# Kernel tuning notes

Measured on AMD Instinct MI355X. Metric: run time of the kernel, lower is better.

## Reference

```python
import jax, jax.numpy as jnp
import numpy as np


def setup_inputs() -> dict:
    key = jax.random.key(0)
    ks = jax.random.split(key, 6)
    B, S, D, H, K = 16384, 16, 256, 128, 32
    s1 = 1.0 / np.sqrt(D)
    s2 = 1.0 / np.sqrt(H)
    s3 = 1.0 / np.sqrt(K)
    return {
        "x": jax.random.normal(ks[0], (B, D), jnp.float32),
        "W1": jax.random.normal(ks[1], (S, D, H), jnp.float32) * s1,
        "b1": jnp.zeros((S, H), jnp.float32),
        "W2": jax.random.normal(ks[2], (S, H, D), jnp.float32) * s2,
        "b2": jnp.zeros((S, D), jnp.float32),
        "Wc1": jax.random.normal(ks[3], (S, D, K), jnp.float32) * s1,
        "bc1": jnp.zeros((S, K), jnp.float32),
        "Wc2": jax.random.normal(ks[4], (S, K), jnp.float32) * s3,
        "bc2": jnp.zeros((S,), jnp.float32),
        "lam": jnp.ones((S,), jnp.float32) / S,  # lambda_weights init = 1/n_sources
    }


def reference(x, W1, b1, W2, b2, Wc1, bc1, Wc2, bc2, lam):
    # Batched per-source 2-layer MLP: [B,D] x [S,D,H] -> [B,S,H]
    h = jax.nn.relu(jnp.einsum("bd,sdh->bsh", x, W1) + b1[None])
    outs = jnp.einsum("bsh,shd->bsd", h, W2) + b2[None]            # [B,S,D]
    # Confidence net on each source output
    ch = jax.nn.relu(jnp.einsum("bsd,sdk->bsk", outs, Wc1) + bc1[None])
    conf = jax.nn.sigmoid(jnp.einsum("bsk,sk->bs", ch, Wc2) + bc2[None])  # [B,S]
    # Weighted, normalized combination
    cw = lam[None, :] * conf                                        # [B,S]
    cw = cw / (cw.sum(axis=1, keepdims=True) + 1e-6)
    out = jnp.einsum("bsd,bs->bd", outs, cw)                        # [B,D]
    return out
```

## Files before the change

kernel.cpp:

```cpp
#include <hip/hip_runtime.h>
#include <math.h>

#define S_N 16
#define D_N 256
#define H_N 128
#define K_N 32
#define BT  64
#define B_N 16384

typedef __attribute__((ext_vector_type(8))) short bf16x8;
typedef __attribute__((ext_vector_type(4))) float f32x4;

#define MFMA(a, b, c) __builtin_amdgcn_mfma_f32_16x16x32_bf16(a, b, c, 0, 0, 0)

static __device__ __forceinline__ unsigned short f2bf(float f) {
  union { float f; unsigned u; } v; v.f = f;
  unsigned r = v.u + 0x7FFFu + ((v.u >> 16) & 1u);
  return (unsigned short)(r >> 16);
}

__global__ __launch_bounds__(256)
void lsi_prep(const float* __restrict__ W1, const float* __restrict__ W2,
              const float* __restrict__ Wc1, const float* __restrict__ b2,
              const float* __restrict__ bc1,
              unsigned short* __restrict__ W1t,
              unsigned short* __restrict__ W2t,
              unsigned short* __restrict__ Wft,
              float* __restrict__ bcf)
{
  const int bid = blockIdx.x;
  if (bid < 1024) {
    __shared__ float t[32][33];
    const float* src; unsigned short* dst; int R, C, r0, c0;
    if (bid < 512) {
      int s = bid >> 5, tt = bid & 31;
      R = 256; C = 128; r0 = (tt >> 2) * 32; c0 = (tt & 3) * 32;
      src = W1 + (size_t)s * 256 * 128; dst = W1t + (size_t)s * 128 * 256;
    } else {
      int s = (bid - 512) >> 5, tt = (bid - 512) & 31;
      R = 128; C = 256; r0 = (tt >> 3) * 32; c0 = (tt & 7) * 32;
      src = W2 + (size_t)s * 128 * 256; dst = W2t + (size_t)s * 256 * 128;
    }
    int li = threadIdx.x >> 5, lj = threadIdx.x & 31;
    #pragma unroll
    for (int i = 0; i < 4; ++i)
      t[li + i * 8][lj] = src[(size_t)(r0 + li + i * 8) * C + c0 + lj];
    __syncthreads();
    #pragma unroll
    for (int i = 0; i < 4; ++i)
      dst[(size_t)(c0 + li + i * 8) * R + r0 + lj] = f2bf(t[lj][li + i * 8]);
    return;
  }
  const int q  = bid - 1024;
  const int s  = q >> 3, hb = q & 7;
  const int t  = threadIdx.x;
  const int hh = hb * 16 + (t >> 4);
  const int kb = (t & 15) * 2;
  const float* w2r = W2 + ((size_t)s * H_N + hh) * D_N;
  const float* wc1 = Wc1 + (size_t)s * D_N * K_N;
  float a0 = 0.f, a1 = 0.f;
  for (int d = 0; d < D_N; ++d) {
    float wv = w2r[d];
    a0 = fmaf(wv, wc1[d * K_N + kb], a0);
    a1 = fmaf(wv, wc1[d * K_N + kb + 1], a1);
  }
  Wft[((size_t)s * K_N + kb) * H_N + hh]     = f2bf(a0);
  Wft[((size_t)s * K_N + kb + 1) * H_N + hh] = f2bf(a1);
  if (hb == 0 && t < K_N) {
    float a = bc1[s * K_N + t];
    for (int d = 0; d < D_N; ++d)
      a = fmaf(b2[s * D_N + d], wc1[d * K_N + t], a);
    bcf[s * K_N + t] = a;
  }
}

template<int SPLIT>
__global__ __launch_bounds__(512, 2)
void lsi_main(const float* __restrict__ x,
              const float* __restrict__ b1,
              const float* __restrict__ b2,
              const float* __restrict__ Wc2,
              const float* __restrict__ bc2,
              const float* __restrict__ lam,
              const unsigned short* __restrict__ W1t,
              const unsigned short* __restrict__ W2t,
              const unsigned short* __restrict__ Wft,
              const float* __restrict__ bcf,
              float* __restrict__ outp,
              float* __restrict__ pwsum)
{
  __shared__ unsigned short x_lds[BT * D_N];
  __shared__ unsigned short h_lds[BT * H_N];
  __shared__ float cw_lds[BT];
  __shared__ float wsum_lds[BT];

  const int tid = threadIdx.x;
  const int w   = tid >> 6;
  const int l   = tid & 63;
  const int rA  = l & 15;
  const int g   = l >> 4;
  const int k8  = g * 8;

  int rb, half, s0, ns;
  if (SPLIT) { rb = blockIdx.x & 255; half = blockIdx.x >> 8; s0 = half * 8; ns = 8; }
  else       { rb = blockIdx.x;       half = 0;               s0 = 0;        ns = 16; }
  const int b0 = rb * BT;

  {
    int row = tid >> 3;
    int c0  = (tid & 7) * 32;
    const float* xr = x + (size_t)(b0 + row) * D_N + c0;
    #pragma unroll
    for (int cc = 0; cc < 4; ++cc) {
      float4 f0 = *(const float4*)(xr + cc * 8);
      float4 f1 = *(const float4*)(xr + cc * 8 + 4);
      bf16x8 u;
      u[0] = f2bf(f0.x); u[1] = f2bf(f0.y); u[2] = f2bf(f0.z); u[3] = f2bf(f0.w);
      u[4] = f2bf(f1.x); u[5] = f2bf(f1.y); u[6] = f2bf(f1.z); u[7] = f2bf(f1.w);
      unsigned off = (unsigned)(row * 512 + (c0 + cc * 8) * 2) ^ (unsigned)((row & 7) << 4);
      *(bf16x8*)((char*)x_lds + off) = u;
    }
  }
  if (tid < BT) wsum_lds[tid] = 0.f;

  f32x4 out_acc[2][4];
  f32x4 acc2[2][4];
  #pragma unroll
  for (int a = 0; a < 2; ++a)
    #pragma unroll
    for (int b = 0; b < 4; ++b)
      out_acc[a][b] = (f32x4){0.f, 0.f, 0.f, 0.f};

  __syncthreads();

  for (int si = 0; si < ns; ++si) {
    const int s = s0 + si;

    f32x4 acc1[4];
    #pragma unroll
    for (int rt = 0; rt < 4; ++rt) acc1[rt] = (f32x4){0.f, 0.f, 0.f, 0.f};
    {
      const unsigned short* B1 = W1t + ((size_t)s * H_N + w * 16 + rA) * D_N + k8;
      #pragma unroll
      for (int ks = 0; ks < 8; ++ks) {
        bf16x8 bfr = *(const bf16x8*)(B1 + ks * 32);
        #pragma unroll
        for (int rt = 0; rt < 4; ++rt) {
          int row = rt * 16 + rA;
          unsigned off = (unsigned)(row * 512 + (ks * 32 + k8) * 2) ^ (unsigned)((row & 7) << 4);
          bf16x8 afr = *(const bf16x8*)((const char*)x_lds + off);
          acc1[rt] = MFMA(afr, bfr, acc1[rt]);
        }
      }
    }
    if (si > 0) {
      #pragma unroll
      for (int rt = 0; rt < 4; ++rt) {
        f32x4 c4 = *(const f32x4*)&cw_lds[rt * 16 + g * 4];
        #pragma unroll
        for (int i = 0; i < 4; ++i) {
          out_acc[0][rt][i] += c4[i] * acc2[0][rt][i];
          out_acc[1][rt][i] += c4[i] * acc2[1][rt][i];
        }
      }
    }
    {
      const float b1v = b1[s * H_N + w * 16 + rA];
      #pragma unroll
      for (int rt = 0; rt < 4; ++rt)
        #pragma unroll
        for (int i = 0; i < 4; ++i) {
          float v = fmaxf(acc1[rt][i] + b1v, 0.f);
          int row = rt * 16 + g * 4 + i;
          unsigned off = (unsigned)(row * 256 + (w * 16 + rA) * 2) ^ (unsigned)((row & 7) << 4);
          *(unsigned short*)((char*)h_lds + off) = f2bf(v);
        }
    }
    __syncthreads();

    if (w < 4) {
      f32x4 acc3[2];
      acc3[0] = (f32x4){0.f, 0.f, 0.f, 0.f};
      acc3[1] = (f32x4){0.f, 0.f, 0.f, 0.f};
      const unsigned short* Bf = Wft + ((size_t)s * K_N + rA) * H_N + k8;
      #pragma unroll
      for (int ks = 0; ks < 4; ++ks) {
        int row = w * 16 + rA;
        unsigned off = (unsigned)(row * 256 + (ks * 32 + k8) * 2) ^ (unsigned)((row & 7) << 4);
        bf16x8 afr = *(const bf16x8*)((const char*)h_lds + off);
        acc3[0] = MFMA(afr, *(const bf16x8*)(Bf + ks * 32), acc3[0]);
        acc3[1] = MFMA(afr, *(const bf16x8*)(Bf + 16 * H_N + ks * 32), acc3[1]);
      }
      const float bcf0 = bcf[s * K_N + rA],      bcf1 = bcf[s * K_N + 16 + rA];
      const float wc20 = Wc2[s * K_N + rA],      wc21 = Wc2[s * K_N + 16 + rA];
      float pz[4];
      #pragma unroll
      for (int i = 0; i < 4; ++i)
        pz[i] = fmaxf(acc3[0][i] + bcf0, 0.f) * wc20 +
                fmaxf(acc3[1][i] + bcf1, 0.f) * wc21;
      #pragma unroll
      for (int m = 1; m < 16; m <<= 1)
        #pragma unroll
        for (int i = 0; i < 4; ++i)
          pz[i] += __shfl_xor(pz[i], m);
      if (rA == 0) {
        const float lam_s = lam[s], bc2_s = bc2[s];
        #pragma unroll
        for (int i = 0; i < 4; ++i) {
          float cv = lam_s / (1.f + __expf(-(pz[i] + bc2_s)));
          cw_lds[w * 16 + g * 4 + i] = cv;
          wsum_lds[w * 16 + g * 4 + i] += cv;
        }
      }
    }

    #pragma unroll
    for (int a = 0; a < 2; ++a)
      #pragma unroll
      for (int b = 0; b < 4; ++b)
        acc2[a][b] = (f32x4){0.f, 0.f, 0.f, 0.f};
    {
      const unsigned short* B2 = W2t + ((size_t)s * D_N + w * 32 + rA) * H_N + k8;
      #pragma unroll
      for (int ks = 0; ks < 4; ++ks) {
        bf16x8 afr[4];
        #pragma unroll
        for (int rt = 0; rt < 4; ++rt) {
          int row = rt * 16 + rA;
          unsigned off = (unsigned)(row * 256 + (ks * 32 + k8) * 2) ^ (unsigned)((row & 7) << 4);
          afr[rt] = *(const bf16x8*)((const char*)h_lds + off);
        }
        #pragma unroll
        for (int ct = 0; ct < 2; ++ct) {
          bf16x8 bfr = *(const bf16x8*)(B2 + ct * 16 * H_N + ks * 32);
          #pragma unroll
          for (int rt = 0; rt < 4; ++rt)
            acc2[ct][rt] = MFMA(afr[rt], bfr, acc2[ct][rt]);
        }
      }
    }
    {
      float b2v0 = b2[s * D_N + w * 32 + rA];
      float b2v1 = b2[s * D_N + w * 32 + 16 + rA];
      #pragma unroll
      for (int rt = 0; rt < 4; ++rt)
        #pragma unroll
        for (int i = 0; i < 4; ++i) {
          acc2[0][rt][i] += b2v0;
          acc2[1][rt][i] += b2v1;
        }
    }
    __syncthreads();
  }

  #pragma unroll
  for (int rt = 0; rt < 4; ++rt) {
    f32x4 c4 = *(const f32x4*)&cw_lds[rt * 16 + g * 4];
    #pragma unroll
    for (int i = 0; i < 4; ++i) {
      out_acc[0][rt][i] += c4[i] * acc2[0][rt][i];
      out_acc[1][rt][i] += c4[i] * acc2[1][rt][i];
    }
  }
  if (SPLIT) {
    float* po = outp + (size_t)half * B_N * D_N;
    #pragma unroll
    for (int rt = 0; rt < 4; ++rt)
      #pragma unroll
      for (int i = 0; i < 4; ++i) {
        int row = rt * 16 + g * 4 + i;
        po[(size_t)(b0 + row) * D_N + w * 32 + rA]      = out_acc[0][rt][i];
        po[(size_t)(b0 + row) * D_N + w * 32 + 16 + rA] = out_acc[1][rt][i];
      }
    if (tid < BT) pwsum[half * B_N + b0 + tid] = wsum_lds[tid];
  } else {
    #pragma unroll
    for (int rt = 0; rt < 4; ++rt) {
      f32x4 w4 = *(const f32x4*)&wsum_lds[rt * 16 + g * 4];
      #pragma unroll
      for (int i = 0; i < 4; ++i) {
        int row = rt * 16 + g * 4 + i;
        float winv = 1.f / (w4[i] + 1e-6f);
        outp[(size_t)(b0 + row) * D_N + w * 32 + rA]      = out_acc[0][rt][i] * winv;
        outp[(size_t)(b0 + row) * D_N + w * 32 + 16 + rA] = out_acc[1][rt][i] * winv;
      }
    }
  }
}

__global__ __launch_bounds__(256)
void lsi_combine(const float* __restrict__ pout, const float* __restrict__ pwsum,
                 float* __restrict__ out)
{
  size_t i4 = ((size_t)blockIdx.x * 256 + threadIdx.x) * 4;
  int row = (int)(i4 >> 8);
  f32x4 a = *(const f32x4*)(pout + i4);
  f32x4 b = *(const f32x4*)(pout + (size_t)B_N * D_N + i4);
  float ws = pwsum[row] + pwsum[B_N + row];
  float inv = 1.f / (ws + 1e-6f);
  f32x4 r;
  #pragma unroll
  for (int i = 0; i < 4; ++i) r[i] = (a[i] + b[i]) * inv;
  *(f32x4*)(out + i4) = r;
}

extern "C" void kernel_launch(void* const* d_in, const int* in_sizes, int n_in,
                              void* d_out, int out_size, void* d_ws, size_t ws_size,
                              hipStream_t stream) {
  const float* x   = (const float*)d_in[0];
  const float* W1  = (const float*)d_in[1];
  const float* b1  = (const float*)d_in[2];
  const float* W2  = (const float*)d_in[3];
  const float* b2  = (const float*)d_in[4];
  const float* Wc1 = (const float*)d_in[5];
  const float* bc1 = (const float*)d_in[6];
  const float* Wc2 = (const float*)d_in[7];
  const float* bc2 = (const float*)d_in[8];
  const float* lam = (const float*)d_in[9];
  float* out = (float*)d_out;

  unsigned short* W1t = (unsigned short*)d_ws;
  unsigned short* W2t = W1t + (size_t)S_N * H_N * D_N;
  unsigned short* Wft = W2t + (size_t)S_N * D_N * H_N;
  float* bcf   = (float*)(Wft + (size_t)S_N * K_N * H_N);
  float* pwsum = bcf + S_N * K_N;
  float* pout  = pwsum + 2 * B_N;
  size_t need = (size_t)((char*)(pout + (size_t)2 * B_N * D_N) - (char*)d_ws);

  lsi_prep<<<dim3(1152), dim3(256), 0, stream>>>(W1, W2, Wc1, b2, bc1,
                                                 W1t, W2t, Wft, bcf);
  if (ws_size >= need) {
    lsi_main<1><<<dim3(512), dim3(512), 0, stream>>>(x, b1, b2, Wc2, bc2, lam,
                                                     W1t, W2t, Wft, bcf, pout, pwsum);
    lsi_combine<<<dim3((B_N * D_N) / 1024), dim3(256), 0, stream>>>(pout, pwsum, out);
  } else {
    lsi_main<0><<<dim3(256), dim3(512), 0, stream>>>(x, b1, b2, Wc2, bc2, lam,
                                                     W1t, W2t, Wft, bcf, out, nullptr);
  }
}
```

Before: 133.2 us.

## Halve batch tile to 32 rows with 256-thread blocks and wider per-wave column tiles

The batch tile drops from 64 to 32 rows and blocks shrink from 8 to 4 waves, with the grid doubled. Each wave now covers twice as many H and D columns: 32 H columns in the first GEMM and 64 D columns in the second. The confidence net runs on 2 waves instead of 4. The goal is smaller blocks and more of them, giving finer scheduling and more resident blocks per CU. The cost is that every bf16 weight matrix is streamed from cache by twice as many blocks, and each B fragment is reused across fewer row tiles.

```diff
diff --git a/kernel.cpp b/kernel.cpp
--- a/kernel.cpp
+++ b/kernel.cpp
@@ -5,7 +5,7 @@
 #define D_N 256
 #define H_N 128
 #define K_N 32
-#define BT  64
+#define BT  32
 #define B_N 16384
 
 typedef __attribute__((ext_vector_type(8))) short bf16x8;
@@ -75,7 +75,7 @@
 }
 
 template<int SPLIT>
-__global__ __launch_bounds__(512, 2)
+__global__ __launch_bounds__(256, 4)
 void lsi_main(const float* __restrict__ x,
               const float* __restrict__ b1,
               const float* __restrict__ b2,
@@ -102,7 +102,7 @@
   const int k8  = g * 8;
 
   int rb, half, s0, ns;
-  if (SPLIT) { rb = blockIdx.x & 255; half = blockIdx.x >> 8; s0 = half * 8; ns = 8; }
+  if (SPLIT) { rb = blockIdx.x & 511; half = blockIdx.x >> 9; s0 = half * 8; ns = 8; }
   else       { rb = blockIdx.x;       half = 0;               s0 = 0;        ns = 16; }
   const int b0 = rb * BT;
 
@@ -123,12 +123,12 @@
   }
   if (tid < BT) wsum_lds[tid] = 0.f;
 
-  f32x4 out_acc[2][4];
-  f32x4 acc2[2][4];
+  f32x4 out_acc[4][2];
+  f32x4 acc2[4][2];
   #pragma unroll
-  for (int a = 0; a < 2; ++a)
-    #pragma unroll
-    for (int b = 0; b < 4; ++b)
+  for (int a = 0; a < 4; ++a)
+    #pragma unroll
+    for (int b = 0; b < 2; ++b)
       out_acc[a][b] = (f32x4){0.f, 0.f, 0.f, 0.f};
 
   __syncthreads();
@@ -136,49 +136,57 @@
   for (int si = 0; si < ns; ++si) {
     const int s = s0 + si;
 
-    f32x4 acc1[4];
-    #pragma unroll
-    for (int rt = 0; rt < 4; ++rt) acc1[rt] = (f32x4){0.f, 0.f, 0.f, 0.f};
+    f32x4 acc1[2][2];
+    #pragma unroll
+    for (int a = 0; a < 2; ++a)
+      #pragma unroll
+      for (int b = 0; b < 2; ++b)
+        acc1[a][b] = (f32x4){0.f, 0.f, 0.f, 0.f};
     {
-      const unsigned short* B1 = W1t + ((size_t)s * H_N + w * 16 + rA) * D_N + k8;
+      const unsigned short* B1 = W1t + ((size_t)s * H_N + w * 32 + rA) * D_N + k8;
       #pragma unroll
       for (int ks = 0; ks < 8; ++ks) {
-        bf16x8 bfr = *(const bf16x8*)(B1 + ks * 32);
-        #pragma unroll
-        for (int rt = 0; rt < 4; ++rt) {
+        bf16x8 bf0 = *(const bf16x8*)(B1 + ks * 32);
+        bf16x8 bf1 = *(const bf16x8*)(B1 + 16 * D_N + ks * 32);
+        #pragma unroll
+        for (int rt = 0; rt < 2; ++rt) {
           int row = rt * 16 + rA;
           unsigned off = (unsigned)(row * 512 + (ks * 32 + k8) * 2) ^ (unsigned)((row & 7) << 4);
           bf16x8 afr = *(const bf16x8*)((const char*)x_lds + off);
-          acc1[rt] = MFMA(afr, bfr, acc1[rt]);
+          acc1[0][rt] = MFMA(afr, bf0, acc1[0][rt]);
+          acc1[1][rt] = MFMA(afr, bf1, acc1[1][rt]);
         }
       }
     }
     if (si > 0) {
       #pragma unroll
-      for (int rt = 0; rt < 4; ++rt) {
+      for (int rt = 0; rt < 2; ++rt) {
         f32x4 c4 = *(const f32x4*)&cw_lds[rt * 16 + g * 4];
         #pragma unroll
-        for (int i = 0; i < 4; ++i) {
-          out_acc[0][rt][i] += c4[i] * acc2[0][rt][i];
-          out_acc[1][rt][i] += c4[i] * acc2[1][rt][i];
-        }
+        for (int ct = 0; ct < 4; ++ct)
+          #pragma unroll
+          for (int i = 0; i < 4; ++i)
+            out_acc[ct][rt][i] += c4[i] * acc2[ct][rt][i];
       }
     }
     {
-      const float b1v = b1[s * H_N + w * 16 + rA];
-      #pragma unroll
-      for (int rt = 0; rt < 4; ++rt)
-        #pragma unroll
-        for (int i = 0; i < 4; ++i) {
-          float v = fmaxf(acc1[rt][i] + b1v, 0.f);
-          int row = rt * 16 + g * 4 + i;
-          unsigned off = (unsigned)(row * 256 + (w * 16 + rA) * 2) ^ (unsigned)((row & 7) << 4);
-          *(unsigned short*)((char*)h_lds + off) = f2bf(v);
-        }
+      const float bv0 = b1[s * H_N + w * 32 + rA];
+      const float bv1 = b1[s * H_N + w * 32 + 16 + rA];
+      #pragma unroll
+      for (int ct = 0; ct < 2; ++ct)
+        #pragma unroll
+        for (int rt = 0; rt < 2; ++rt)
+          #pragma unroll
+          for (int i = 0; i < 4; ++i) {
+            float v = fmaxf(acc1[ct][rt][i] + (ct ? bv1 : bv0), 0.f);
+            int row = rt * 16 + g * 4 + i;
+            unsigned off = (unsigned)(row * 256 + (w * 32 + ct * 16 + rA) * 2) ^ (unsigned)((row & 7) << 4);
+            *(unsigned short*)((char*)h_lds + off) = f2bf(v);
+          }
     }
     __syncthreads();
 
-    if (w < 4) {
+    if (w < 2) {
       f32x4 acc3[2];
       acc3[0] = (f32x4){0.f, 0.f, 0.f, 0.f};
       acc3[1] = (f32x4){0.f, 0.f, 0.f, 0.f};
@@ -215,74 +223,76 @@
     }
 
     #pragma unroll
-    for (int a = 0; a < 2; ++a)
-      #pragma unroll
-      for (int b = 0; b < 4; ++b)
+    for (int a = 0; a < 4; ++a)
+      #pragma unroll
+      for (int b = 0; b < 2; ++b)
         acc2[a][b] = (f32x4){0.f, 0.f, 0.f, 0.f};
     {
-      const unsigned short* B2 = W2t + ((size_t)s * D_N + w * 32 + rA) * H_N + k8;
+      const unsigned short* B2 = W2t + ((size_t)s * D_N + w * 64 + rA) * H_N + k8;
       #pragma unroll
       for (int ks = 0; ks < 4; ++ks) {
-        bf16x8 afr[4];
-        #pragma unroll
-        for (int rt = 0; rt < 4; ++rt) {
+        bf16x8 afr[2];
+        #pragma unroll
+        for (int rt = 0; rt < 2; ++rt) {
           int row = rt * 16 + rA;
           unsigned off = (unsigned)(row * 256 + (ks * 32 + k8) * 2) ^ (unsigned)((row & 7) << 4);
           afr[rt] = *(const bf16x8*)((const char*)h_lds + off);
         }
         #pragma unroll
-        for (int ct = 0; ct < 2; ++ct) {
+        for (int ct = 0; ct < 4; ++ct) {
           bf16x8 bfr = *(const bf16x8*)(B2 + ct * 16 * H_N + ks * 32);
           #pragma unroll
-          for (int rt = 0; rt < 4; ++rt)
+          for (int rt = 0; rt < 2; ++rt)
             acc2[ct][rt] = MFMA(afr[rt], bfr, acc2[ct][rt]);
         }
       }
     }
     {
-      float b2v0 = b2[s * D_N + w * 32 + rA];
-      float b2v1 = b2[s * D_N + w * 32 + 16 + rA];
-      #pragma unroll
-      for (int rt = 0; rt < 4; ++rt)
-        #pragma unroll
-        for (int i = 0; i < 4; ++i) {
-          acc2[0][rt][i] += b2v0;
-          acc2[1][rt][i] += b2v1;
-        }
+      #pragma unroll
+      for (int ct = 0; ct < 4; ++ct) {
+        float b2v = b2[s * D_N + w * 64 + ct * 16 + rA];
+        #pragma unroll
+        for (int rt = 0; rt < 2; ++rt)
+          #pragma unroll
+          for (int i = 0; i < 4; ++i)
+            acc2[ct][rt][i] += b2v;
+      }
     }
     __syncthreads();
   }
 
   #pragma unroll
-  for (int rt = 0; rt < 4; ++rt) {
+  for (int rt = 0; rt < 2; ++rt) {
     f32x4 c4 = *(const f32x4*)&cw_lds[rt * 16 + g * 4];
     #pragma unroll
-    for (int i = 0; i < 4; ++i) {
-      out_acc[0][rt][i] += c4[i] * acc2[0][rt][i];
-      out_acc[1][rt][i] += c4[i] * acc2[1][rt][i];
-    }
+    for (int ct = 0; ct < 4; ++ct)
+      #pragma unroll
+      for (int i = 0; i < 4; ++i)
+        out_acc[ct][rt][i] += c4[i] * acc2[ct][rt][i];
   }
   if (SPLIT) {
     float* po = outp + (size_t)half * B_N * D_N;
     #pragma unroll
-    for (int rt = 0; rt < 4; ++rt)
+    for (int rt = 0; rt < 2; ++rt)
       #pragma unroll
       for (int i = 0; i < 4; ++i) {
         int row = rt * 16 + g * 4 + i;
-        po[(size_t)(b0 + row) * D_N + w * 32 + rA]      = out_acc[0][rt][i];
-        po[(size_t)(b0 + row) * D_N + w * 32 + 16 + rA] = out_acc[1][rt][i];
+        #pragma unroll
+        for (int ct = 0; ct < 4; ++ct)
+          po[(size_t)(b0 + row) * D_N + w * 64 + ct * 16 + rA] = out_acc[ct][rt][i];
       }
     if (tid < BT) pwsum[half * B_N + b0 + tid] = wsum_lds[tid];
   } else {
     #pragma unroll
-    for (int rt = 0; rt < 4; ++rt) {
+    for (int rt = 0; rt < 2; ++rt) {
       f32x4 w4 = *(const f32x4*)&wsum_lds[rt * 16 + g * 4];
       #pragma unroll
       for (int i = 0; i < 4; ++i) {
         int row = rt * 16 + g * 4 + i;
         float winv = 1.f / (w4[i] + 1e-6f);
-        outp[(size_t)(b0 + row) * D_N + w * 32 + rA]      = out_acc[0][rt][i] * winv;
-        outp[(size_t)(b0 + row) * D_N + w * 32 + 16 + rA] = out_acc[1][rt][i] * winv;
+        #pragma unroll
+        for (int ct = 0; ct < 4; ++ct)
+          outp[(size_t)(b0 + row) * D_N + w * 64 + ct * 16 + rA] = out_acc[ct][rt][i] * winv;
       }
     }
   }
@@ -330,11 +340,11 @@
   lsi_prep<<<dim3(1152), dim3(256), 0, stream>>>(W1, W2, Wc1, b2, bc1,
                                                  W1t, W2t, Wft, bcf);
   if (ws_size >= need) {
-    lsi_main<1><<<dim3(512), dim3(512), 0, stream>>>(x, b1, b2, Wc2, bc2, lam,
-                                                     W1t, W2t, Wft, bcf, pout, pwsum);
+    lsi_main<1><<<dim3(1024), dim3(256), 0, stream>>>(x, b1, b2, Wc2, bc2, lam,
+                                                      W1t, W2t, Wft, bcf, pout, pwsum);
     lsi_combine<<<dim3((B_N * D_N) / 1024), dim3(256), 0, stream>>>(pout, pwsum, out);
   } else {
-    lsi_main<0><<<dim3(256), dim3(512), 0, stream>>>(x, b1, b2, Wc2, bc2, lam,
+    lsi_main<0><<<dim3(512), dim3(256), 0, stream>>>(x, b1, b2, Wc2, bc2, lam,
                                                      W1t, W2t, Wft, bcf, out, nullptr);
   }
 }
```

New measurement: 191.2 us. 43.5% more time.

## Double-buffer hidden activations and drop source split with combine kernel

Applied to the files above, without the earlier changes.

Removes the two-way source split, its partial-output buffers and the separate combine kernel, so each block processes all 16 sources and writes normalized output directly. The hidden-activation and confidence-weight LDS buffers are double-buffered so the first GEMM for the next source runs in the same phase as the confidence and second GEMM for the current source, leaving one barrier per source instead of two. This avoids writing and rereading two full partial outputs, but halves the grid to 256 blocks, which may leave compute units underused, and LDS use per block grows.

```diff
diff --git a/kernel.cpp b/kernel.cpp
--- a/kernel.cpp
+++ b/kernel.cpp
@@ -74,7 +74,6 @@
   }
 }
 
-template<int SPLIT>
 __global__ __launch_bounds__(512, 2)
 void lsi_main(const float* __restrict__ x,
               const float* __restrict__ b1,
@@ -86,12 +85,11 @@
               const unsigned short* __restrict__ W2t,
               const unsigned short* __restrict__ Wft,
               const float* __restrict__ bcf,
-              float* __restrict__ outp,
-              float* __restrict__ pwsum)
+              float* __restrict__ out)
 {
   __shared__ unsigned short x_lds[BT * D_N];
-  __shared__ unsigned short h_lds[BT * H_N];
-  __shared__ float cw_lds[BT];
+  __shared__ unsigned short h_lds[2][BT * H_N];
+  __shared__ float cw_lds[2][BT];
   __shared__ float wsum_lds[BT];
 
   const int tid = threadIdx.x;
@@ -100,11 +98,7 @@
   const int rA  = l & 15;
   const int g   = l >> 4;
   const int k8  = g * 8;
-
-  int rb, half, s0, ns;
-  if (SPLIT) { rb = blockIdx.x & 255; half = blockIdx.x >> 8; s0 = half * 8; ns = 8; }
-  else       { rb = blockIdx.x;       half = 0;               s0 = 0;        ns = 16; }
-  const int b0 = rb * BT;
+  const int b0  = blockIdx.x * BT;
 
   {
     int row = tid >> 3;
@@ -131,32 +125,45 @@
     for (int b = 0; b < 4; ++b)
       out_acc[a][b] = (f32x4){0.f, 0.f, 0.f, 0.f};
 
+  auto do_gemm1 = [&](int s, unsigned short* hw) {
+    f32x4 acc1[4];
+    #pragma unroll
+    for (int rt = 0; rt < 4; ++rt) acc1[rt] = (f32x4){0.f, 0.f, 0.f, 0.f};
+    const unsigned short* B1 = W1t + ((size_t)s * H_N + w * 16 + rA) * D_N + k8;
+    #pragma unroll
+    for (int ks = 0; ks < 8; ++ks) {
+      bf16x8 bfr = *(const bf16x8*)(B1 + ks * 32);
+      #pragma unroll
+      for (int rt = 0; rt < 4; ++rt) {
+        int row = rt * 16 + rA;
+        unsigned off = (unsigned)(row * 512 + (ks * 32 + k8) * 2) ^ (unsigned)((row & 7) << 4);
+        bf16x8 afr = *(const bf16x8*)((const char*)x_lds + off);
+        acc1[rt] = MFMA(afr, bfr, acc1[rt]);
+      }
+    }
+    const float b1v = b1[s * H_N + w * 16 + rA];
+    #pragma unroll
+    for (int rt = 0; rt < 4; ++rt)
+      #pragma unroll
+      for (int i = 0; i < 4; ++i) {
+        float v = fmaxf(acc1[rt][i] + b1v, 0.f);
+        int row = rt * 16 + g * 4 + i;
+        unsigned off = (unsigned)(row * 256 + (w * 16 + rA) * 2) ^ (unsigned)((row & 7) << 4);
+        *(unsigned short*)((char*)hw + off) = f2bf(v);
+      }
+  };
+
   __syncthreads();
-
-  for (int si = 0; si < ns; ++si) {
-    const int s = s0 + si;
-
-    f32x4 acc1[4];
-    #pragma unroll
-    for (int rt = 0; rt < 4; ++rt) acc1[rt] = (f32x4){0.f, 0.f, 0.f, 0.f};
-    {
-      const unsigned short* B1 = W1t + ((size_t)s * H_N + w * 16 + rA) * D_N + k8;
-      #pragma unroll
-      for (int ks = 0; ks < 8; ++ks) {
-        bf16x8 bfr = *(const bf16x8*)(B1 + ks * 32);
-        #pragma unroll
-        for (int rt = 0; rt < 4; ++rt) {
-          int row = rt * 16 + rA;
-          unsigned off = (unsigned)(row * 512 + (ks * 32 + k8) * 2) ^ (unsigned)((row & 7) << 4);
-          bf16x8 afr = *(const bf16x8*)((const char*)x_lds + off);
-          acc1[rt] = MFMA(afr, bfr, acc1[rt]);
-        }
-      }
-    }
-    if (si > 0) {
+  do_gemm1(0, h_lds[0]);
+  __syncthreads();
+
+  for (int s = 0; s < S_N; ++s) {
+    const unsigned short* hr = (const unsigned short*)h_lds[s & 1];
+
+    if (s > 0) {
       #pragma unroll
       for (int rt = 0; rt < 4; ++rt) {
-        f32x4 c4 = *(const f32x4*)&cw_lds[rt * 16 + g * 4];
+        f32x4 c4 = *(const f32x4*)&cw_lds[(s + 1) & 1][rt * 16 + g * 4];
         #pragma unroll
         for (int i = 0; i < 4; ++i) {
           out_acc[0][rt][i] += c4[i] * acc2[0][rt][i];
@@ -164,19 +171,6 @@
         }
       }
     }
-    {
-      const float b1v = b1[s * H_N + w * 16 + rA];
-      #pragma unroll
-      for (int rt = 0; rt < 4; ++rt)
-        #pragma unroll
-        for (int i = 0; i < 4; ++i) {
-          float v = fmaxf(acc1[rt][i] + b1v, 0.f);
-          int row = rt * 16 + g * 4 + i;
-          unsigned off = (unsigned)(row * 256 + (w * 16 + rA) * 2) ^ (unsigned)((row & 7) << 4);
-          *(unsigned short*)((char*)h_lds + off) = f2bf(v);
-        }
-    }
-    __syncthreads();
 
     if (w < 4) {
       f32x4 acc3[2];
@@ -187,12 +181,12 @@
       for (int ks = 0; ks < 4; ++ks) {
         int row = w * 16 + rA;
         unsigned off = (unsigned)(row * 256 + (ks * 32 + k8) * 2) ^ (unsigned)((row & 7) << 4);
-        bf16x8 afr = *(const bf16x8*)((const char*)h_lds + off);
+        bf16x8 afr = *(const bf16x8*)((const char*)hr + off);
         acc3[0] = MFMA(afr, *(const bf16x8*)(Bf + ks * 32), acc3[0]);
         acc3[1] = MFMA(afr, *(const bf16x8*)(Bf + 16 * H_N + ks * 32), acc3[1]);
       }
-      const float bcf0 = bcf[s * K_N + rA],      bcf1 = bcf[s * K_N + 16 + rA];
-      const float wc20 = Wc2[s * K_N + rA],      wc21 = Wc2[s * K_N + 16 + rA];
+      const float bcf0 = bcf[s * K_N + rA],  bcf1 = bcf[s * K_N + 16 + rA];
+      const float wc20 = Wc2[s * K_N + rA],  wc21 = Wc2[s * K_N + 16 + rA];
       float pz[4];
       #pragma unroll
       for (int i = 0; i < 4; ++i)
@@ -208,7 +202,7 @@
         #pragma unroll
         for (int i = 0; i < 4; ++i) {
           float cv = lam_s / (1.f + __expf(-(pz[i] + bc2_s)));
-          cw_lds[w * 16 + g * 4 + i] = cv;
+          cw_lds[s & 1][w * 16 + g * 4 + i] = cv;
           wsum_lds[w * 16 + g * 4 + i] += cv;
         }
       }
@@ -228,7 +222,7 @@
         for (int rt = 0; rt < 4; ++rt) {
           int row = rt * 16 + rA;
           unsigned off = (unsigned)(row * 256 + (ks * 32 + k8) * 2) ^ (unsigned)((row & 7) << 4);
-          afr[rt] = *(const bf16x8*)((const char*)h_lds + off);
+          afr[rt] = *(const bf16x8*)((const char*)hr + off);
         }
         #pragma unroll
         for (int ct = 0; ct < 2; ++ct) {
@@ -238,8 +232,6 @@
             acc2[ct][rt] = MFMA(afr[rt], bfr, acc2[ct][rt]);
         }
       }
-    }
-    {
       float b2v0 = b2[s * D_N + w * 32 + rA];
       float b2v1 = b2[s * D_N + w * 32 + 16 + rA];
       #pragma unroll
@@ -250,58 +242,32 @@
           acc2[1][rt][i] += b2v1;
         }
     }
+
+    if (s + 1 < S_N) do_gemm1(s + 1, h_lds[(s + 1) & 1]);
+
     __syncthreads();
   }
 
   #pragma unroll
   for (int rt = 0; rt < 4; ++rt) {
-    f32x4 c4 = *(const f32x4*)&cw_lds[rt * 16 + g * 4];
+    f32x4 c4 = *(const f32x4*)&cw_lds[(S_N - 1) & 1][rt * 16 + g * 4];
     #pragma unroll
     for (int i = 0; i < 4; ++i) {
       out_acc[0][rt][i] += c4[i] * acc2[0][rt][i];
       out_acc[1][rt][i] += c4[i] * acc2[1][rt][i];
     }
   }
-  if (SPLIT) {
-    float* po = outp + (size_t)half * B_N * D_N;
-    #pragma unroll
-    for (int rt = 0; rt < 4; ++rt)
-      #pragma unroll
-      for (int i = 0; i < 4; ++i) {
-        int row = rt * 16 + g * 4 + i;
-        po[(size_t)(b0 + row) * D_N + w * 32 + rA]      = out_acc[0][rt][i];
-        po[(size_t)(b0 + row) * D_N + w * 32 + 16 + rA] = out_acc[1][rt][i];
-      }
-    if (tid < BT) pwsum[half * B_N + b0 + tid] = wsum_lds[tid];
-  } else {
-    #pragma unroll
-    for (int rt = 0; rt < 4; ++rt) {
-      f32x4 w4 = *(const f32x4*)&wsum_lds[rt * 16 + g * 4];
-      #pragma unroll
-      for (int i = 0; i < 4; ++i) {
-        int row = rt * 16 + g * 4 + i;
-        float winv = 1.f / (w4[i] + 1e-6f);
-        outp[(size_t)(b0 + row) * D_N + w * 32 + rA]      = out_acc[0][rt][i] * winv;
-        outp[(size_t)(b0 + row) * D_N + w * 32 + 16 + rA] = out_acc[1][rt][i] * winv;
-      }
-    }
-  }
-}
-
-__global__ __launch_bounds__(256)
-void lsi_combine(const float* __restrict__ pout, const float* __restrict__ pwsum,
-                 float* __restrict__ out)
-{
-  size_t i4 = ((size_t)blockIdx.x * 256 + threadIdx.x) * 4;
-  int row = (int)(i4 >> 8);
-  f32x4 a = *(const f32x4*)(pout + i4);
-  f32x4 b = *(const f32x4*)(pout + (size_t)B_N * D_N + i4);
-  float ws = pwsum[row] + pwsum[B_N + row];
-  float inv = 1.f / (ws + 1e-6f);
-  f32x4 r;
   #pragma unroll
-  for (int i = 0; i < 4; ++i) r[i] = (a[i] + b[i]) * inv;
-  *(f32x4*)(out + i4) = r;
+  for (int rt = 0; rt < 4; ++rt) {
+    f32x4 w4 = *(const f32x4*)&wsum_lds[rt * 16 + g * 4];
+    #pragma unroll
+    for (int i = 0; i < 4; ++i) {
+      int row = rt * 16 + g * 4 + i;
+      float winv = 1.f / (w4[i] + 1e-6f);
+      out[(size_t)(b0 + row) * D_N + w * 32 + rA]      = out_acc[0][rt][i] * winv;
+      out[(size_t)(b0 + row) * D_N + w * 32 + 16 + rA] = out_acc[1][rt][i] * winv;
+    }
+  }
 }
 
 extern "C" void kernel_launch(void* const* d_in, const int* in_sizes, int n_in,
@@ -322,19 +288,10 @@
   unsigned short* W1t = (unsigned short*)d_ws;
   unsigned short* W2t = W1t + (size_t)S_N * H_N * D_N;
   unsigned short* Wft = W2t + (size_t)S_N * D_N * H_N;
-  float* bcf   = (float*)(Wft + (size_t)S_N * K_N * H_N);
-  float* pwsum = bcf + S_N * K_N;
-  float* pout  = pwsum + 2 * B_N;
-  size_t need = (size_t)((char*)(pout + (size_t)2 * B_N * D_N) - (char*)d_ws);
+  float* bcf = (float*)(Wft + (size_t)S_N * K_N * H_N);
 
   lsi_prep<<<dim3(1152), dim3(256), 0, stream>>>(W1, W2, Wc1, b2, bc1,
                                                  W1t, W2t, Wft, bcf);
-  if (ws_size >= need) {
-    lsi_main<1><<<dim3(512), dim3(512), 0, stream>>>(x, b1, b2, Wc2, bc2, lam,
-                                                     W1t, W2t, Wft, bcf, pout, pwsum);
-    lsi_combine<<<dim3((B_N * D_N) / 1024), dim3(256), 0, stream>>>(pout, pwsum, out);
-  } else {
-    lsi_main<0><<<dim3(256), dim3(512), 0, stream>>>(x, b1, b2, Wc2, bc2, lam,
-                                                     W1t, W2t, Wft, bcf, out, nullptr);
-  }
-}
+  lsi_main<<<dim3(B_N / BT), dim3(512), 0, stream>>>(x, b1, b2, Wc2, bc2, lam,
+                                                     W1t, W2t, Wft, bcf, out);
+}
```

After: 123.9 us. 7.0% less time.
